# Kernel tuning notes

Hardware: AMD Instinct MI355X
Metric: run time of the kernel (lower is better)

## Reference

```python
import jax, jax.numpy as jnp
import numpy as np

S_DIM, I_DIM, O_DIM = 1024, 2048, 1024
TOTAL = S_DIM + I_DIM + O_DIM  # 4096
INPUT_DIM, NUM_CLASSES, BATCH = 2048, 1000, 256


def setup_inputs() -> dict:
    key = jax.random.key(0)
    ks = jax.random.split(key, 6)
    x = jax.random.normal(ks[0], (BATCH, INPUT_DIM), dtype=jnp.float32)
    W = jax.random.normal(ks[1], (TOTAL, TOTAL), dtype=jnp.float32) * 0.02
    # torch Linear: weight [out, in], bias [out]
    in_w = jax.random.normal(ks[2], (S_DIM, INPUT_DIM), dtype=jnp.float32) * (1.0 / np.sqrt(INPUT_DIM))
    in_b = jax.random.normal(ks[3], (S_DIM,), dtype=jnp.float32) * 0.01
    out_w = jax.random.normal(ks[4], (NUM_CLASSES, O_DIM), dtype=jnp.float32) * (1.0 / np.sqrt(O_DIM))
    out_b = jax.random.normal(ks[5], (NUM_CLASSES,), dtype=jnp.float32) * 0.01
    return {"x": x, "W": W, "in_w": in_w, "in_b": in_b, "out_w": out_w, "out_b": out_b, "time_steps": 10}


def reference(x, W, in_w, in_b, out_w, out_b, time_steps):
    B = x.shape[0]
    S, I, O = S_DIM, I_DIM, O_DIM
    # slice effective W into 9 sub-blocks (use_lora=False -> W_eff = W)
    W_ss, W_sr, W_so = W[:S, :S], W[:S, S:S + I], W[:S, S + I:]
    W_rs, W_rr, W_ro = W[S:S + I, :S], W[S:S + I, S:S + I], W[S:S + I, S + I:]
    W_os, W_or, W_oo = W[S + I:, :S], W[S + I:, S:S + I], W[S + I:, S + I:]

    E = x @ in_w.T + in_b  # [B, S]
    gate = (jnp.arange(time_steps) % 5 == 0).astype(x.dtype)  # E injected when t%5==0

    init = (jnp.zeros((B, S), x.dtype), jnp.zeros((B, I), x.dtype), jnp.zeros((B, O), x.dtype))

    def step(carry, g):
        Ss, Is, Os = carry
        S_next = jax.nn.relu(Ss @ W_ss + g * E + Is @ W_rs + Os @ W_os)
        I_next = jax.nn.relu(Is @ W_rr + Ss @ W_sr + Os @ W_or)
        O_next = jax.nn.relu(Os @ W_oo + Is @ W_ro + Ss @ W_so)
        return (S_next, I_next, O_next), None

    (Ss, Is, Os), _ = jax.lax.scan(step, init, gate)
    return Os @ out_w.T + out_b  # [B, num_classes]
```

## Files before the change

### kernel.cpp

```cpp
#include <hip/hip_runtime.h>


typedef __bf16 bf16x8 __attribute__((ext_vector_type(8)));
typedef float  f32x16 __attribute__((ext_vector_type(16)));

#define TOTAL 4096
#define BATCH 256
#define INDIM 2048
#define SDIM  1024
#define NCLS  1000

#define MFMA(a, b, c) __builtin_amdgcn_mfma_f32_32x32x16_bf16((a), (b), (c), 0, 0, 0)

__device__ inline f32x16 zero16() {
    f32x16 v;
#pragma unroll
    for (int i = 0; i < 16; ++i) v[i] = 0.f;
    return v;
}

__device__ inline void swz_slot(const float* __restrict__ in, __bf16* __restrict__ out,
                                int C, int Rvalid, int t) {
    const int lane = t & 63;
    const int frag = t >> 6;
    const int kcN = C >> 4;
    const int rt = frag / kcN;
    const int kc = frag - rt * kcN;
    const int r = rt * 32 + (lane & 31);
    const int c = kc * 16 + (lane >> 5) * 8;
    alignas(16) __bf16 v[8];
    if (r < Rvalid) {
        const float* p = in + (size_t)r * C + c;
#pragma unroll
        for (int j = 0; j < 8; ++j) v[j] = (__bf16)p[j];
    } else {
#pragma unroll
        for (int j = 0; j < 8; ++j) v[j] = (__bf16)0.f;
    }
    *(ulonglong2*)(out + (size_t)t * 8) = *(const ulonglong2*)v;
}

__global__ __launch_bounds__(256) void k_prep(const float* __restrict__ W,
                                              const float* __restrict__ x,
                                              const float* __restrict__ in_w,
                                              const float* __restrict__ in_b,
                                              const float* __restrict__ out_w,
                                              __bf16* __restrict__ WT,
                                              __bf16* __restrict__ OWT,
                                              float* __restrict__ Ebuf,
                                              __bf16* __restrict__ H0) {
    __shared__ float t[16 * 512];
    const int bid = blockIdx.x;
    const int tid = threadIdx.x;
    if (bid < 256) {
        float* red = t;
        const int mt = bid >> 5, nt = bid & 31;
        const int wave = tid >> 6, lane = tid & 63;
        const int l31 = lane & 31, kh = (lane >> 5) * 8;
        const int k0 = wave * 512;
        const float* Ax = x    + (size_t)(mt * 32 + l31) * INDIM + k0 + kh;
        const float* Bw = in_w + (size_t)(nt * 32 + l31) * INDIM + k0 + kh;
        f32x16 acc = zero16();
#pragma unroll 4
        for (int i = 0; i < 32; ++i) {
            const float* pa = Ax + i * 16;
            const float* pb = Bw + i * 16;
            float4 a0 = *(const float4*)pa, a1 = *(const float4*)(pa + 4);
            float4 b0 = *(const float4*)pb, b1 = *(const float4*)(pb + 4);
            bf16x8 a, b;
            a[0] = (__bf16)a0.x; a[1] = (__bf16)a0.y; a[2] = (__bf16)a0.z; a[3] = (__bf16)a0.w;
            a[4] = (__bf16)a1.x; a[5] = (__bf16)a1.y; a[6] = (__bf16)a1.z; a[7] = (__bf16)a1.w;
            b[0] = (__bf16)b0.x; b[1] = (__bf16)b0.y; b[2] = (__bf16)b0.z; b[3] = (__bf16)b0.w;
            b[4] = (__bf16)b1.x; b[5] = (__bf16)b1.y; b[6] = (__bf16)b1.z; b[7] = (__bf16)b1.w;
            acc = MFMA(a, b, acc);
        }
#pragma unroll
        for (int r = 0; r < 16; ++r) {
            int row = (r & 3) + 8 * (r >> 2) + 4 * (lane >> 5);
            red[wave * 1024 + row * 32 + l31] = acc[r];
        }
        __syncthreads();
        const int e0 = tid * 4;
        float4 s = {0.f, 0.f, 0.f, 0.f};
#pragma unroll
        for (int w = 0; w < 4; ++w) {
            float4 v = *(const float4*)&red[w * 1024 + e0];
            s.x += v.x; s.y += v.y; s.z += v.z; s.w += v.w;
        }
        const int row = e0 >> 5, col = e0 & 31;
        const int m = mt * 32 + row, n = nt * 32 + col;
        float v[4] = {s.x + in_b[n], s.y + in_b[n + 1], s.z + in_b[n + 2], s.w + in_b[n + 3]};
        *(float4*)(Ebuf + m * SDIM + n) = *(const float4*)v;
        alignas(8) __bf16 o[4];
#pragma unroll
        for (int j = 0; j < 4; ++j) o[j] = (__bf16)fmaxf(v[j], 0.f);
        const size_t frag = (size_t)(m >> 5) * (TOTAL / 16) + (n >> 4);
        const int lh = (m & 31) + 32 * ((n >> 3) & 1);
        *(ushort4*)(H0 + frag * 512 + lh * 8 + (n & 7)) = *(const ushort4*)o;
    } else if (bid < 2304) {
        const int wb = bid - 256;
        const int k0 = (wb >> 3) * 16;
        const int n0 = (wb & 7) * 512;
#pragma unroll
        for (int i = 0; i < 8; ++i) {
            const int slot = i * 256 + tid;
            const int row = slot >> 7;
            const int c4 = (slot & 127) * 4;
            float4 v = *(const float4*)(W + (size_t)(k0 + row) * TOTAL + n0 + c4);
            *(float4*)&t[row * 512 + c4] = v;
        }
        __syncthreads();
        const int kcG = k0 >> 4;
#pragma unroll
        for (int s = tid; s < 1024; s += 256) {
            const int rtl = s >> 6;
            const int lane = s & 63;
            const int nl = rtl * 32 + (lane & 31);
            const int kl = (lane >> 5) * 8;
            bf16x8 v;
#pragma unroll
            for (int j = 0; j < 8; ++j) v[j] = (__bf16)t[(kl + j) * 512 + nl];
            const size_t fragG = (size_t)((n0 >> 5) + rtl) * (TOTAL / 16) + kcG;
            *(bf16x8*)(WT + fragG * 512 + lane * 8) = v;
        }
    } else {
        swz_slot(out_w, OWT, 1024, NCLS, (bid - 2304) * 256 + tid);
    }
}

template <int CHUNKS>
__global__ __launch_bounds__(512, 2) void k_step(const __bf16* __restrict__ h,
                                                 const __bf16* __restrict__ WT,
                                                 const float* __restrict__ E,
                                                 const int gate,
                                                 __bf16* __restrict__ hn) {
    __shared__ float buf[4][4096];
    const int wave = threadIdx.x >> 6;
    const int lane = threadIdx.x & 63;
    const int xcd = blockIdx.x & 7;
    const int idx = blockIdx.x >> 3;
    const int mt = idx & 3;
    const int nt = xcd * 8 + (idx >> 2);
    constexpr int PER = CHUNKS >> 3;
    const int kc0 = wave * PER;

    const bf16x8* A0 = (const bf16x8*)h  + ((size_t)(mt * 2) * (TOTAL / 16) + kc0) * 64 + lane;
    const bf16x8* A1 = A0 + (size_t)(TOTAL / 16) * 64;
    const bf16x8* B0 = (const bf16x8*)WT + ((size_t)(nt * 2) * (TOTAL / 16) + kc0) * 64 + lane;
    const bf16x8* B1 = B0 + (size_t)(TOTAL / 16) * 64;

    f32x16 ac0 = zero16(), ac1 = zero16(), ac2 = zero16(), ac3 = zero16();
#pragma unroll 4
    for (int i = 0; i < PER; ++i) {
        const int off = i * 64;
        bf16x8 a0 = A0[off];
        bf16x8 a1 = A1[off];
        bf16x8 b0 = B0[off];
        bf16x8 b1 = B1[off];
        ac0 = MFMA(a0, b0, ac0);
        ac1 = MFMA(a0, b1, ac1);
        ac2 = MFMA(a1, b0, ac2);
        ac3 = MFMA(a1, b1, ac3);
    }

    f32x16 accs[4] = {ac0, ac1, ac2, ac3};
    if (wave >= 4) {
        float* b = buf[wave - 4];
#pragma unroll
        for (int c = 0; c < 4; ++c)
#pragma unroll
            for (int r = 0; r < 16; ++r)
                b[(c * 16 + r) * 64 + lane] = accs[c][r];
    }
    __syncthreads();
    if (wave < 4) {
        float* b = buf[wave];
#pragma unroll
        for (int c = 0; c < 4; ++c)
#pragma unroll
            for (int r = 0; r < 16; ++r) {
                const int i2 = (c * 16 + r) * 64 + lane;
                b[i2] += accs[c][r];
            }
    }
    __syncthreads();

    const int t = threadIdx.x;
    const int c = t >> 7;
    const int r = (t >> 3) & 15;
    const int l0 = (t & 7) * 8;
    const int base = (c * 16 + r) * 64 + l0;
    float4 s0 = {0.f, 0.f, 0.f, 0.f}, s1 = {0.f, 0.f, 0.f, 0.f};
#pragma unroll
    for (int w = 0; w < 4; ++w) {
        const float4* p = (const float4*)&buf[w][base];
        float4 v0 = p[0], v1 = p[1];
        s0.x += v0.x; s0.y += v0.y; s0.z += v0.z; s0.w += v0.w;
        s1.x += v1.x; s1.y += v1.y; s1.z += v1.z; s1.w += v1.w;
    }
    float v[8] = {s0.x, s0.y, s0.z, s0.w, s1.x, s1.y, s1.z, s1.w};
    const int ih = c >> 1, jh = c & 1;
    const int row = ih * 32 + (r & 3) + 8 * (r >> 2) + 4 * (l0 >> 5);
    const int col0 = jh * 32 + (l0 & 31);
    const int m = mt * 64 + row;
    const int n0g = nt * 64 + col0;
    if (gate && n0g < SDIM) {
        const float* Ep = E + m * SDIM + n0g;
#pragma unroll
        for (int j = 0; j < 8; ++j) v[j] += Ep[j];
    }
    alignas(16) __bf16 o[8];
#pragma unroll
    for (int j = 0; j < 8; ++j) o[j] = (__bf16)fmaxf(v[j], 0.f);
    const size_t frag = (size_t)(m >> 5) * (TOTAL / 16) + (n0g >> 4);
    const int lh = (m & 31) + 32 * ((n0g >> 3) & 1);
    *(ulonglong2*)(hn + frag * 512 + lh * 8) = *(const ulonglong2*)o;
}

__global__ __launch_bounds__(512, 4) void k_out(const __bf16* __restrict__ h,
                                                const __bf16* __restrict__ owt,
                                                const float* __restrict__ out_b,
                                                float* __restrict__ out) {
    __shared__ float red[8][1024];
    const int wave = threadIdx.x >> 6;
    const int lane = threadIdx.x & 63;
    const int mt = blockIdx.x >> 5;
    const int ct = blockIdx.x & 31;
    const int m0 = mt * 32, c0 = ct * 32;
    const int kcA0 = (3072 / 16) + wave * 8;
    const int kcB0 = wave * 8;
    const bf16x8* Ap = (const bf16x8*)h   + ((size_t)mt * (TOTAL / 16) + kcA0) * 64 + lane;
    const bf16x8* Bp = (const bf16x8*)owt + ((size_t)ct * (1024 / 16) + kcB0) * 64 + lane;
    f32x16 acc = zero16();
#pragma unroll
    for (int i = 0; i < 8; ++i)
        acc = MFMA(Ap[i * 64], Bp[i * 64], acc);
#pragma unroll
    for (int r = 0; r < 16; ++r) {
        int row = (r & 3) + 8 * (r >> 2) + 4 * (lane >> 5);
        red[wave][row * 32 + (lane & 31)] = acc[r];
    }
    __syncthreads();
    const int e0 = threadIdx.x * 2;
    float sx = 0.f, sy = 0.f;
#pragma unroll
    for (int w = 0; w < 8; ++w) {
        float2 v = *(const float2*)&red[w][e0];
        sx += v.x; sy += v.y;
    }
    const int row = e0 >> 5, col = e0 & 31;
    const int m = m0 + row;
    const int n = c0 + col;
    if (n < NCLS)     out[m * NCLS + n]     = sx + out_b[n];
    if (n + 1 < NCLS) out[m * NCLS + n + 1] = sy + out_b[n + 1];
}

extern "C" void kernel_launch(void* const* d_in, const int* in_sizes, int n_in,
                              void* d_out, int out_size, void* d_ws, size_t ws_size,
                              hipStream_t stream) {
    const float* x     = (const float*)d_in[0];
    const float* W     = (const float*)d_in[1];
    const float* in_w  = (const float*)d_in[2];
    const float* in_b  = (const float*)d_in[3];
    const float* out_w = (const float*)d_in[4];
    const float* out_b = (const float*)d_in[5];
    float* out = (float*)d_out;

    char* ws = (char*)d_ws;
    __bf16* WT  = (__bf16*)(ws + 0);
    __bf16* OWT = (__bf16*)(ws + 33554432);
    float*  Ebuf= (float*)(ws + 35651584);
    __bf16* H0  = (__bf16*)(ws + 36700160);
    __bf16* H1  = (__bf16*)(ws + 38797312);

    k_prep<<<2816, 256, 0, stream>>>(W, x, in_w, in_b, out_w, WT, OWT, Ebuf, H0);

    const __bf16* hs = H0;
    __bf16* hd = H1;
    for (int t = 1; t < 10; ++t) {
        const int gate = (t % 5 == 0) ? 1 : 0;
        if (t == 1)
            k_step<SDIM / 16><<<256, 512, 0, stream>>>(hs, WT, Ebuf, gate, hd);
        else
            k_step<TOTAL / 16><<<256, 512, 0, stream>>>(hs, WT, Ebuf, gate, hd);
        const __bf16* tmp = hs; hs = hd; hd = (__bf16*)tmp;
    }

    k_out<<<256, 512, 0, stream>>>(hs, OWT, out_b, out);
}
```

Measured before the change: 263.6 us.

## Stage step GEMM operands through LDS with double-buffered async global loads

Rewrites the recurrent step kernel so each block streams 8 K-chunks of A and B per iteration into LDS with global_load_lds, double-buffering across iterations. Each wave then owns one 32x32 output quadrant and half of each chunk's K range, replacing the per-wave 64x64 K-split with direct global loads and the 4-way reduction. The intent is to share operand loads across waves and overlap memory with MFMA. In exchange it adds a __syncthreads per chunk and only one MFMA accumulator per wave, so there is less independent MFMA work to hide latency. The gate flag also becomes a template parameter.

```diff
diff --git a/kernel.cpp b/kernel.cpp
--- a/kernel.cpp
+++ b/kernel.cpp
@@ -9,6 +9,7 @@
 #define INDIM 2048
 #define SDIM  1024
 #define NCLS  1000
+#define KC    (TOTAL / 16)
 
 #define MFMA(a, b, c) __builtin_amdgcn_mfma_f32_32x32x16_bf16((a), (b), (c), 0, 0, 0)
 
@@ -17,6 +18,12 @@
 #pragma unroll
     for (int i = 0; i < 16; ++i) v[i] = 0.f;
     return v;
+}
+
+__device__ inline void gload16(const __bf16* g, __bf16* l) {
+    __builtin_amdgcn_global_load_lds(
+        (const __attribute__((address_space(1))) void*)g,
+        (__attribute__((address_space(3))) void*)l, 16, 0, 0);
 }
 
 __device__ inline void swz_slot(const float* __restrict__ in, __bf16* __restrict__ out,
@@ -94,7 +101,7 @@
         alignas(8) __bf16 o[4];
 #pragma unroll
         for (int j = 0; j < 4; ++j) o[j] = (__bf16)fmaxf(v[j], 0.f);
-        const size_t frag = (size_t)(m >> 5) * (TOTAL / 16) + (n >> 4);
+        const size_t frag = (size_t)(m >> 5) * KC + (n >> 4);
         const int lh = (m & 31) + 32 * ((n >> 3) & 1);
         *(ushort4*)(H0 + frag * 512 + lh * 8 + (n & 7)) = *(const ushort4*)o;
     } else if (bid < 2304) {
@@ -120,7 +127,7 @@
             bf16x8 v;
 #pragma unroll
             for (int j = 0; j < 8; ++j) v[j] = (__bf16)t[(kl + j) * 512 + nl];
-            const size_t fragG = (size_t)((n0 >> 5) + rtl) * (TOTAL / 16) + kcG;
+            const size_t fragG = (size_t)((n0 >> 5) + rtl) * KC + kcG;
             *(bf16x8*)(WT + fragG * 512 + lane * 8) = v;
         }
     } else {
@@ -128,83 +135,88 @@
     }
 }
 
-template <int CHUNKS>
+template <int NC, int GATE>
 __global__ __launch_bounds__(512, 2) void k_step(const __bf16* __restrict__ h,
                                                  const __bf16* __restrict__ WT,
                                                  const float* __restrict__ E,
-                                                 const int gate,
                                                  __bf16* __restrict__ hn) {
-    __shared__ float buf[4][4096];
+    __shared__ __align__(16) char smem[65536];
+    __bf16* As = (__bf16*)smem;
+    __bf16* Bs = (__bf16*)(smem + 32768);
     const int wave = threadIdx.x >> 6;
     const int lane = threadIdx.x & 63;
     const int xcd = blockIdx.x & 7;
     const int idx = blockIdx.x >> 3;
     const int mt = idx & 3;
     const int nt = xcd * 8 + (idx >> 2);
-    constexpr int PER = CHUNKS >> 3;
-    const int kc0 = wave * PER;
-
-    const bf16x8* A0 = (const bf16x8*)h  + ((size_t)(mt * 2) * (TOTAL / 16) + kc0) * 64 + lane;
-    const bf16x8* A1 = A0 + (size_t)(TOTAL / 16) * 64;
-    const bf16x8* B0 = (const bf16x8*)WT + ((size_t)(nt * 2) * (TOTAL / 16) + kc0) * 64 + lane;
-    const bf16x8* B1 = B0 + (size_t)(TOTAL / 16) * 64;
-
-    f32x16 ac0 = zero16(), ac1 = zero16(), ac2 = zero16(), ac3 = zero16();
-#pragma unroll 4
-    for (int i = 0; i < PER; ++i) {
-        const int off = i * 64;
-        bf16x8 a0 = A0[off];
-        bf16x8 a1 = A1[off];
-        bf16x8 b0 = B0[off];
-        bf16x8 b1 = B1[off];
-        ac0 = MFMA(a0, b0, ac0);
-        ac1 = MFMA(a0, b1, ac1);
-        ac2 = MFMA(a1, b0, ac2);
-        ac3 = MFMA(a1, b1, ac3);
-    }
-
-    f32x16 accs[4] = {ac0, ac1, ac2, ac3};
-    if (wave >= 4) {
-        float* b = buf[wave - 4];
-#pragma unroll
-        for (int c = 0; c < 4; ++c)
-#pragma unroll
-            for (int r = 0; r < 16; ++r)
-                b[(c * 16 + r) * 64 + lane] = accs[c][r];
-    }
+
+    const __bf16* pA0 = h  + ((size_t)(mt * 2) * KC + wave) * 512 + lane * 8;
+    const __bf16* pA1 = pA0 + (size_t)KC * 512;
+    const __bf16* pB0 = WT + ((size_t)(nt * 2) * KC + wave) * 512 + lane * 8;
+    const __bf16* pB1 = pB0 + (size_t)KC * 512;
+    __bf16* dA0 = As + wave * 512;
+    __bf16* dA1 = As + (8 + wave) * 512;
+    __bf16* dB0 = Bs + wave * 512;
+    __bf16* dB1 = Bs + (8 + wave) * 512;
+
+    const int q = wave & 3;
+    const int ks = wave >> 2;
+    const int mh = q >> 1, nh = q & 1;
+    const int aoff = mh * 8 * 512 + lane * 8;
+    const int boff = nh * 8 * 512 + lane * 8;
+
+    f32x16 acc = zero16();
+
+    gload16(pA0, dA0); gload16(pA1, dA1);
+    gload16(pB0, dB0); gload16(pB1, dB1);
     __syncthreads();
-    if (wave < 4) {
-        float* b = buf[wave];
-#pragma unroll
-        for (int c = 0; c < 4; ++c)
-#pragma unroll
-            for (int r = 0; r < 16; ++r) {
-                const int i2 = (c * 16 + r) * 64 + lane;
-                b[i2] += accs[c][r];
-            }
+
+    for (int c = 0; c < NC; ++c) {
+        const int cur = (c & 1) * 8192;
+        if (c + 1 < NC) {
+            const size_t go = (size_t)(c + 1) * 4096;
+            const int nb = ((c + 1) & 1) * 8192;
+            gload16(pA0 + go, dA0 + nb); gload16(pA1 + go, dA1 + nb);
+            gload16(pB0 + go, dB0 + nb); gload16(pB1 + go, dB1 + nb);
+        }
+#pragma unroll
+        for (int j = 0; j < 4; ++j) {
+            const int kcl = ks * 4 + j;
+            bf16x8 a = *(const bf16x8*)(As + cur + kcl * 512 + aoff);
+            bf16x8 b = *(const bf16x8*)(Bs + cur + kcl * 512 + boff);
+            acc = MFMA(a, b, acc);
+        }
+        __syncthreads();
+    }
+
+    float* redD = (float*)smem;
+    float* redF = (float*)(smem + 32768);
+    if (ks == 1) {
+#pragma unroll
+        for (int r = 0; r < 16; ++r)
+            redD[(q * 16 + r) * 64 + lane] = acc[r];
     }
     __syncthreads();
+    if (ks == 0) {
+        const int col = nh * 32 + (lane & 31);
+#pragma unroll
+        for (int r = 0; r < 16; ++r) {
+            float s = acc[r] + redD[(q * 16 + r) * 64 + lane];
+            const int row = mh * 32 + (r & 3) + 8 * (r >> 2) + 4 * (lane >> 5);
+            redF[row * 64 + col] = s;
+        }
+    }
+    __syncthreads();
 
     const int t = threadIdx.x;
-    const int c = t >> 7;
-    const int r = (t >> 3) & 15;
-    const int l0 = (t & 7) * 8;
-    const int base = (c * 16 + r) * 64 + l0;
-    float4 s0 = {0.f, 0.f, 0.f, 0.f}, s1 = {0.f, 0.f, 0.f, 0.f};
-#pragma unroll
-    for (int w = 0; w < 4; ++w) {
-        const float4* p = (const float4*)&buf[w][base];
-        float4 v0 = p[0], v1 = p[1];
-        s0.x += v0.x; s0.y += v0.y; s0.z += v0.z; s0.w += v0.w;
-        s1.x += v1.x; s1.y += v1.y; s1.z += v1.z; s1.w += v1.w;
-    }
-    float v[8] = {s0.x, s0.y, s0.z, s0.w, s1.x, s1.y, s1.z, s1.w};
-    const int ih = c >> 1, jh = c & 1;
-    const int row = ih * 32 + (r & 3) + 8 * (r >> 2) + 4 * (l0 >> 5);
-    const int col0 = jh * 32 + (l0 & 31);
+    const int row = t >> 3;
+    const int col0 = (t & 7) * 8;
+    float4 v0 = *(const float4*)&redF[row * 64 + col0];
+    float4 v1 = *(const float4*)&redF[row * 64 + col0 + 4];
+    float v[8] = {v0.x, v0.y, v0.z, v0.w, v1.x, v1.y, v1.z, v1.w};
     const int m = mt * 64 + row;
     const int n0g = nt * 64 + col0;
-    if (gate && n0g < SDIM) {
+    if (GATE && n0g < SDIM) {
         const float* Ep = E + m * SDIM + n0g;
 #pragma unroll
         for (int j = 0; j < 8; ++j) v[j] += Ep[j];
@@ -212,7 +224,7 @@
     alignas(16) __bf16 o[8];
 #pragma unroll
     for (int j = 0; j < 8; ++j) o[j] = (__bf16)fmaxf(v[j], 0.f);
-    const size_t frag = (size_t)(m >> 5) * (TOTAL / 16) + (n0g >> 4);
+    const size_t frag = (size_t)(m >> 5) * KC + (n0g >> 4);
     const int lh = (m & 31) + 32 * ((n0g >> 3) & 1);
     *(ulonglong2*)(hn + frag * 512 + lh * 8) = *(const ulonglong2*)o;
 }
@@ -229,7 +241,7 @@
     const int m0 = mt * 32, c0 = ct * 32;
     const int kcA0 = (3072 / 16) + wave * 8;
     const int kcB0 = wave * 8;
-    const bf16x8* Ap = (const bf16x8*)h   + ((size_t)mt * (TOTAL / 16) + kcA0) * 64 + lane;
+    const bf16x8* Ap = (const bf16x8*)h   + ((size_t)mt * KC + kcA0) * 64 + lane;
     const bf16x8* Bp = (const bf16x8*)owt + ((size_t)ct * (1024 / 16) + kcB0) * 64 + lane;
     f32x16 acc = zero16();
 #pragma unroll
@@ -278,11 +290,12 @@
     const __bf16* hs = H0;
     __bf16* hd = H1;
     for (int t = 1; t < 10; ++t) {
-        const int gate = (t % 5 == 0) ? 1 : 0;
         if (t == 1)
-            k_step<SDIM / 16><<<256, 512, 0, stream>>>(hs, WT, Ebuf, gate, hd);
+            k_step<8, 0><<<256, 512, 0, stream>>>(hs, WT, Ebuf, hd);
+        else if (t == 5)
+            k_step<32, 1><<<256, 512, 0, stream>>>(hs, WT, Ebuf, hd);
         else
-            k_step<TOTAL / 16><<<256, 512, 0, stream>>>(hs, WT, Ebuf, gate, hd);
+            k_step<32, 0><<<256, 512, 0, stream>>>(hs, WT, Ebuf, hd);
         const __bf16* tmp = hs; hs = hd; hd = (__bf16*)tmp;
     }
 
```

Result: slower. 295.1 us (+11.9%).
